# Kernel tuning notes

Measured on AMD Instinct MI355X. Metric: run time of the kernel, lower is better.

The kernel has to match this reference:

```python
import jax, jax.numpy as jnp
import numpy as np

B, T, D, UNITS = 32, 2048, 1024, 1024


def setup_inputs() -> dict:
    key = jax.random.key(0)
    ks = jax.random.split(key, 9)
    values = jax.random.normal(ks[0], (B, T, D), dtype=jnp.float32)
    query = jax.random.normal(ks[1], (B, D), dtype=jnp.float32)
    # mask: 1.0 where position is masked out, 0.0 otherwise
    mask = jax.random.randint(ks[2], (B, T), 0, 2).astype(jnp.float32)
    # Dense params (keras Dense: y = x @ W + b)
    W1 = jax.random.normal(ks[3], (D, UNITS), dtype=jnp.float32) / np.sqrt(D)
    b1 = jnp.zeros((UNITS,), dtype=jnp.float32)
    W2 = jax.random.normal(ks[4], (D, UNITS), dtype=jnp.float32) / np.sqrt(D)
    b2 = jnp.zeros((UNITS,), dtype=jnp.float32)
    V = jax.random.normal(ks[5], (UNITS, 1), dtype=jnp.float32) / np.sqrt(UNITS)
    bV = jnp.zeros((1,), dtype=jnp.float32)
    return {"values": values, "query": query, "mask": mask,
            "W1": W1, "b1": b1, "W2": W2, "b2": b2, "V": V, "bV": bV}


def reference(values, query, mask, W1, b1, W2, b2, V, bV):
    # values: [B,T,D], query: [B,D], mask: [B,T] (1.0 = masked)
    proj_v = jnp.einsum('btd,du->btu', values, W1) + b1          # [B,T,U]
    proj_q = (query @ W2 + b2)[:, None, :]                        # [B,1,U]
    score = jnp.tanh(proj_v + proj_q) @ V + bV                    # [B,T,1]
    score = score + mask[:, :, None] * (-1e9)                     # mask out
    attention_weights = jax.nn.softmax(score, axis=1)             # [B,T,1]
    context_vector = jnp.sum(attention_weights * values, axis=1)  # [B,D]
    return (context_vector, attention_weights)
```

## Files before the change

kernel.cpp:

```cpp
#include <hip/hip_runtime.h>
#include <hip/hip_bf16.h>


typedef __bf16 bf16x8 __attribute__((ext_vector_type(8)));
typedef __bf16 bf16x4 __attribute__((ext_vector_type(4)));
typedef float  f32x4  __attribute__((ext_vector_type(4)));

#define B_  32
#define T_  2048
#define D_  1024
#define U_  1024

#define WS_W1T    ((size_t)0)
#define WS_PROJQ  ((size_t)(2u*1024*1024))
#define WS_SCORE  ((size_t)(2u*1024*1024 + 128u*1024))

__global__ void init_kernel(const float* __restrict__ b1, const float* __restrict__ b2,
                            float* __restrict__ projq, float* __restrict__ score) {
    int i = blockIdx.x * 256 + threadIdx.x;
    if (i < B_ * U_) {
        projq[i] = b1[i & (U_ - 1)] + b2[i & (U_ - 1)];
    } else {
        score[i - B_ * U_] = 0.0f;
    }
}

__global__ void w1_transpose_kernel(const float* __restrict__ W1, __bf16* __restrict__ W1T) {
    __shared__ float tile[64][65];
    const int bx = blockIdx.x & 15;
    const int by = blockIdx.x >> 4;
    const int tid = threadIdx.x;
    const int j  = tid & 63;
    const int i0 = tid >> 6;
#pragma unroll
    for (int p = 0; p < 16; ++p) {
        const int i = i0 + p * 4;
        tile[i][j] = W1[(size_t)(by * 64 + i) * U_ + bx * 64 + j];
    }
    __syncthreads();
#pragma unroll
    for (int p = 0; p < 16; ++p) {
        const int i = i0 + p * 4;
        W1T[(size_t)(bx * 64 + i) * D_ + by * 64 + j] = (__bf16)tile[j][i];
    }
}

__global__ void projq_kernel(const float* __restrict__ query, const float* __restrict__ W2,
                             float* __restrict__ projq) {
    __shared__ float q[128];
    const int b  = blockIdx.x >> 3;
    const int dc = blockIdx.x & 7;
    const int tid = threadIdx.x;
    if (tid < 128) q[tid] = query[(size_t)b * D_ + dc * 128 + tid];
    __syncthreads();
    const int u0 = tid * 4;
    float a0 = 0.f, a1 = 0.f, a2 = 0.f, a3 = 0.f;
    for (int d = 0; d < 128; ++d) {
        const float4 w = *(const float4*)(W2 + (size_t)(dc * 128 + d) * U_ + u0);
        const float qd = q[d];
        a0 = fmaf(qd, w.x, a0); a1 = fmaf(qd, w.y, a1);
        a2 = fmaf(qd, w.z, a2); a3 = fmaf(qd, w.w, a3);
    }
    float* p = projq + (size_t)b * U_ + u0;
    atomicAdd(p + 0, a0); atomicAdd(p + 1, a1);
    atomicAdd(p + 2, a2); atomicAdd(p + 3, a3);
}

__global__ __launch_bounds__(512, 2)
void score_kernel(const float* __restrict__ values, const __bf16* __restrict__ W1T,
                  const float* __restrict__ projq, const float* __restrict__ V,
                  float* __restrict__ score) {
    __shared__ __attribute__((aligned(16))) __bf16 Al[64][40];
    __shared__ __attribute__((aligned(16))) __bf16 Bl[512][40];

    const int tid    = threadIdx.x;
    const int rowblk = blockIdx.x >> 1;
    const int nhalf  = blockIdx.x & 1;
    const int wave = tid >> 6, lane = tid & 63;
    const int quad = lane >> 4, l15 = lane & 15;

    const float*  Abase = values + (size_t)rowblk * 64 * D_;
    const __bf16* Bbase = W1T + (size_t)nhalf * 512 * D_;

    const int ar = tid >> 3;
    const int ac = (tid & 7) * 4;
    const int br = tid >> 2;
    const int bc = (tid & 3) * 8;

    f32x4 acc[4][4];
#pragma unroll
    for (int i = 0; i < 4; ++i)
#pragma unroll
        for (int j = 0; j < 4; ++j) {
            f32x4 z = {0.f, 0.f, 0.f, 0.f};
            acc[i][j] = z;
        }

    for (int kk = 0; kk < D_; kk += 32) {
        {
            const float4 v = *(const float4*)(Abase + (size_t)ar * D_ + kk + ac);
            bf16x4 h;
            h[0] = (__bf16)v.x; h[1] = (__bf16)v.y; h[2] = (__bf16)v.z; h[3] = (__bf16)v.w;
            *(bf16x4*)(&Al[ar][ac]) = h;
        }
#pragma unroll
        for (int p = 0; p < 4; ++p) {
            const int rr = p * 128 + br;
            const bf16x8 w = *(const bf16x8*)(Bbase + (size_t)rr * D_ + kk + bc);
            *(bf16x8*)(&Bl[rr][bc]) = w;
        }
        __syncthreads();

        bf16x8 af[4];
#pragma unroll
        for (int mt = 0; mt < 4; ++mt)
            af[mt] = *(const bf16x8*)(&Al[mt * 16 + l15][quad * 8]);
#pragma unroll
        for (int nt = 0; nt < 4; ++nt) {
            const bf16x8 bfr = *(const bf16x8*)(&Bl[wave * 64 + nt * 16 + l15][quad * 8]);
#pragma unroll
            for (int mt = 0; mt < 4; ++mt)
                acc[mt][nt] = __builtin_amdgcn_mfma_f32_16x16x32_bf16(af[mt], bfr, acc[mt][nt], 0, 0, 0);
        }
        __syncthreads();
    }

    const int b = rowblk >> 5;
    const size_t rowbase = (size_t)rowblk * 64;
    const float* pq = projq + (size_t)b * U_;
    const int ub = nhalf * 512 + wave * 64;
#pragma unroll
    for (int mt = 0; mt < 4; ++mt) {
        float s0 = 0.f, s1 = 0.f, s2 = 0.f, s3 = 0.f;
#pragma unroll
        for (int nt = 0; nt < 4; ++nt) {
            const int u = ub + nt * 16 + l15;
            const float pqu = pq[u];
            const float vu  = V[u];
            s0 += tanhf(acc[mt][nt][0] + pqu) * vu;
            s1 += tanhf(acc[mt][nt][1] + pqu) * vu;
            s2 += tanhf(acc[mt][nt][2] + pqu) * vu;
            s3 += tanhf(acc[mt][nt][3] + pqu) * vu;
        }
        float s[4] = {s0, s1, s2, s3};
#pragma unroll
        for (int r = 0; r < 4; ++r) {
            float v = s[r];
            v += __shfl_xor(v, 1);
            v += __shfl_xor(v, 2);
            v += __shfl_xor(v, 4);
            v += __shfl_xor(v, 8);
            if (l15 == 0)
                atomicAdd(&score[rowbase + mt * 16 + quad * 4 + r], v);
        }
    }
}

__global__ void softmax_kernel(const float* __restrict__ score, const float* __restrict__ mask,
                               const float* __restrict__ bV, float* __restrict__ out) {
    const int b = blockIdx.x;
    const int tid = threadIdx.x;
    const float bv = bV[0];
    float s[8];
    float lmax = -3.0e38f;
#pragma unroll
    for (int i = 0; i < 8; ++i) {
        const int t = tid + i * 256;
        const float v = score[(size_t)b * T_ + t] + bv + mask[(size_t)b * T_ + t] * (-1.0e9f);
        s[i] = v;
        lmax = fmaxf(lmax, v);
    }
#pragma unroll
    for (int m = 1; m < 64; m <<= 1) lmax = fmaxf(lmax, __shfl_xor(lmax, m));
    __shared__ float redm[4], reds[4];
    if ((tid & 63) == 0) redm[tid >> 6] = lmax;
    __syncthreads();
    const float M = fmaxf(fmaxf(redm[0], redm[1]), fmaxf(redm[2], redm[3]));
    float lsum = 0.f;
#pragma unroll
    for (int i = 0; i < 8; ++i) { s[i] = __expf(s[i] - M); lsum += s[i]; }
#pragma unroll
    for (int m = 1; m < 64; m <<= 1) lsum += __shfl_xor(lsum, m);
    if ((tid & 63) == 0) reds[tid >> 6] = lsum;
    __syncthreads();
    const float inv = 1.0f / (reds[0] + reds[1] + reds[2] + reds[3]);
#pragma unroll
    for (int i = 0; i < 8; ++i)
        out[(size_t)B_ * D_ + (size_t)b * T_ + tid + i * 256] = s[i] * inv;
}

__global__ void context_kernel(const float* __restrict__ values, const float* __restrict__ attn,
                               float* __restrict__ out) {
    const int b  = blockIdx.x >> 4;
    const int dc = blockIdx.x & 15;
    const int tid = threadIdx.x;
    __shared__ float a[T_];
#pragma unroll
    for (int i = 0; i < 8; ++i) a[tid + i * 256] = attn[(size_t)b * T_ + tid + i * 256];
    __syncthreads();
    const int d  = dc * 64 + (tid & 63);
    const int tg = tid >> 6;
    const float* vb = values + (size_t)b * T_ * D_ + d;
    float acc = 0.f;
#pragma unroll 4
    for (int t = tg; t < T_; t += 4)
        acc = fmaf(a[t], vb[(size_t)t * D_], acc);
    __shared__ float red[4][64];
    red[tg][tid & 63] = acc;
    __syncthreads();
    if (tid < 64)
        out[(size_t)b * D_ + dc * 64 + tid] = red[0][tid] + red[1][tid] + red[2][tid] + red[3][tid];
}

extern "C" void kernel_launch(void* const* d_in, const int* in_sizes, int n_in,
                              void* d_out, int out_size, void* d_ws, size_t ws_size,
                              hipStream_t stream) {
    const float* values = (const float*)d_in[0];
    const float* query  = (const float*)d_in[1];
    const float* mask   = (const float*)d_in[2];
    const float* W1     = (const float*)d_in[3];
    const float* b1     = (const float*)d_in[4];
    const float* W2     = (const float*)d_in[5];
    const float* b2     = (const float*)d_in[6];
    const float* V      = (const float*)d_in[7];
    const float* bV     = (const float*)d_in[8];
    float* out = (float*)d_out;

    char* ws = (char*)d_ws;
    __bf16* W1T  = (__bf16*)(ws + WS_W1T);
    float*  projq = (float*)(ws + WS_PROJQ);
    float*  score = (float*)(ws + WS_SCORE);

    init_kernel<<<dim3(384), dim3(256), 0, stream>>>(b1, b2, projq, score);
    w1_transpose_kernel<<<dim3(256), dim3(256), 0, stream>>>(W1, W1T);
    projq_kernel<<<dim3(256), dim3(256), 0, stream>>>(query, W2, projq);
    score_kernel<<<dim3(2048), dim3(512), 0, stream>>>(values, W1T, projq, V, score);
    softmax_kernel<<<dim3(32), dim3(256), 0, stream>>>(score, mask, bV, out);
    context_kernel<<<dim3(512), dim3(256), 0, stream>>>(values, out + B_ * D_, out);
}
```

Measured before the change: 714.3 us.

## Pre-convert values to bf16, retile score GEMM with direct-to-LDS loads, fast tanh

Adds a conversion pass that writes values as bf16 into workspace, then runs a new 128x128-tile score GEMM that loads A and B straight into LDS with global_load_lds. The previous f32-input kernel is kept as a fallback for when the workspace is too small. tanhf is replaced by an exp-based approximation. The context kernel is vectorised to float4 loads with 16 t-groups. The extra conversion pass adds a full read of values and a 128MB write, and the new path depends on the workspace size, which is not shown.

```diff
diff --git a/kernel.cpp b/kernel.cpp
--- a/kernel.cpp
+++ b/kernel.cpp
@@ -10,10 +10,24 @@
 #define T_  2048
 #define D_  1024
 #define U_  1024
+#define BT_ (B_*T_)
 
 #define WS_W1T    ((size_t)0)
 #define WS_PROJQ  ((size_t)(2u*1024*1024))
 #define WS_SCORE  ((size_t)(2u*1024*1024 + 128u*1024))
+#define WS_VALB   ((size_t)(4u*1024*1024))
+#define WS_NEEDED (WS_VALB + (size_t)BT_ * D_ * 2)
+
+__device__ __forceinline__ float tanh_fast(float x) {
+    const float e = __expf(2.0f * x);
+    return 1.0f - __fdividef(2.0f, e + 1.0f);
+}
+
+__device__ __forceinline__ void glls16(const void* g, void* l) {
+    __builtin_amdgcn_global_load_lds(
+        (const __attribute__((address_space(1))) void*)g,
+        (__attribute__((address_space(3))) void*)l, 16, 0, 0);
+}
 
 __global__ void init_kernel(const float* __restrict__ b1, const float* __restrict__ b2,
                             float* __restrict__ projq, float* __restrict__ score) {
@@ -25,6 +39,16 @@
     }
 }
 
+__global__ void convert_kernel(const float* __restrict__ v, __bf16* __restrict__ o) {
+    const size_t i = ((size_t)blockIdx.x * 256 + threadIdx.x) * 8;
+    const float4 a = *(const float4*)(v + i);
+    const float4 b = *(const float4*)(v + i + 4);
+    bf16x8 h;
+    h[0] = (__bf16)a.x; h[1] = (__bf16)a.y; h[2] = (__bf16)a.z; h[3] = (__bf16)a.w;
+    h[4] = (__bf16)b.x; h[5] = (__bf16)b.y; h[6] = (__bf16)b.z; h[7] = (__bf16)b.w;
+    *(bf16x8*)(o + i) = h;
+}
+
 __global__ void w1_transpose_kernel(const float* __restrict__ W1, __bf16* __restrict__ W1T) {
     __shared__ float tile[64][65];
     const int bx = blockIdx.x & 15;
@@ -66,26 +90,25 @@
     atomicAdd(p + 2, a2); atomicAdd(p + 3, a3);
 }
 
-__global__ __launch_bounds__(512, 2)
-void score_kernel(const float* __restrict__ values, const __bf16* __restrict__ W1T,
-                  const float* __restrict__ projq, const float* __restrict__ V,
-                  float* __restrict__ score) {
-    __shared__ __attribute__((aligned(16))) __bf16 Al[64][40];
-    __shared__ __attribute__((aligned(16))) __bf16 Bl[512][40];
-
-    const int tid    = threadIdx.x;
-    const int rowblk = blockIdx.x >> 1;
-    const int nhalf  = blockIdx.x & 1;
+__global__ __launch_bounds__(256, 3)
+void score_kernel_bf16(const __bf16* __restrict__ valb, const __bf16* __restrict__ W1T,
+                       const float* __restrict__ projq, const float* __restrict__ V,
+                       float* __restrict__ score) {
+    __shared__ __attribute__((aligned(16))) __bf16 Al[128 * 32];
+    __shared__ __attribute__((aligned(16))) __bf16 Bl[128 * 32];
+
+    const int tid = threadIdx.x;
+    const int rowblk = blockIdx.x >> 3;
+    const int utile  = blockIdx.x & 7;
     const int wave = tid >> 6, lane = tid & 63;
     const int quad = lane >> 4, l15 = lane & 15;
-
-    const float*  Abase = values + (size_t)rowblk * 64 * D_;
-    const __bf16* Bbase = W1T + (size_t)nhalf * 512 * D_;
-
-    const int ar = tid >> 3;
-    const int ac = (tid & 7) * 4;
-    const int br = tid >> 2;
-    const int bc = (tid & 3) * 8;
+    const int wr = (wave >> 1) * 64;
+    const int wc = (wave & 1) * 64;
+
+    const __bf16* Ab = valb + ((size_t)rowblk * 128 + (tid >> 2)) * D_ + (tid & 3) * 8;
+    const __bf16* Bb = W1T + ((size_t)utile * 128 + (tid >> 2)) * D_ + (tid & 3) * 8;
+    __bf16* Ald = Al + wave * 512;
+    __bf16* Bld = Bl + wave * 512;
 
     f32x4 acc[4][4];
 #pragma unroll
@@ -97,27 +120,19 @@
         }
 
     for (int kk = 0; kk < D_; kk += 32) {
-        {
-            const float4 v = *(const float4*)(Abase + (size_t)ar * D_ + kk + ac);
-            bf16x4 h;
-            h[0] = (__bf16)v.x; h[1] = (__bf16)v.y; h[2] = (__bf16)v.z; h[3] = (__bf16)v.w;
-            *(bf16x4*)(&Al[ar][ac]) = h;
-        }
-#pragma unroll
-        for (int p = 0; p < 4; ++p) {
-            const int rr = p * 128 + br;
-            const bf16x8 w = *(const bf16x8*)(Bbase + (size_t)rr * D_ + kk + bc);
-            *(bf16x8*)(&Bl[rr][bc]) = w;
-        }
+        glls16(Ab + kk,            Ald);
+        glls16(Ab + 64 * D_ + kk,  Ald + 2048);
+        glls16(Bb + kk,            Bld);
+        glls16(Bb + 64 * D_ + kk,  Bld + 2048);
         __syncthreads();
 
         bf16x8 af[4];
 #pragma unroll
         for (int mt = 0; mt < 4; ++mt)
-            af[mt] = *(const bf16x8*)(&Al[mt * 16 + l15][quad * 8]);
+            af[mt] = *(const bf16x8*)(Al + (wr + mt * 16 + l15) * 32 + quad * 8);
 #pragma unroll
         for (int nt = 0; nt < 4; ++nt) {
-            const bf16x8 bfr = *(const bf16x8*)(&Bl[wave * 64 + nt * 16 + l15][quad * 8]);
+            const bf16x8 bfr = *(const bf16x8*)(Bl + (wc + nt * 16 + l15) * 32 + quad * 8);
 #pragma unroll
             for (int mt = 0; mt < 4; ++mt)
                 acc[mt][nt] = __builtin_amdgcn_mfma_f32_16x16x32_bf16(af[mt], bfr, acc[mt][nt], 0, 0, 0);
@@ -125,22 +140,22 @@
         __syncthreads();
     }
 
-    const int b = rowblk >> 5;
-    const size_t rowbase = (size_t)rowblk * 64;
-    const float* pq = projq + (size_t)b * U_;
-    const int ub = nhalf * 512 + wave * 64;
+    const int b = rowblk >> 4;
+    const float* pq = projq + (size_t)b * U_ + utile * 128 + wc;
+    const float* Vp = V + utile * 128 + wc;
+    const size_t rowbase = (size_t)rowblk * 128 + wr;
 #pragma unroll
     for (int mt = 0; mt < 4; ++mt) {
         float s0 = 0.f, s1 = 0.f, s2 = 0.f, s3 = 0.f;
 #pragma unroll
         for (int nt = 0; nt < 4; ++nt) {
-            const int u = ub + nt * 16 + l15;
+            const int u = nt * 16 + l15;
             const float pqu = pq[u];
-            const float vu  = V[u];
-            s0 += tanhf(acc[mt][nt][0] + pqu) * vu;
-            s1 += tanhf(acc[mt][nt][1] + pqu) * vu;
-            s2 += tanhf(acc[mt][nt][2] + pqu) * vu;
-            s3 += tanhf(acc[mt][nt][3] + pqu) * vu;
+            const float vu  = Vp[u];
+            s0 += tanh_fast(acc[mt][nt][0] + pqu) * vu;
+            s1 += tanh_fast(acc[mt][nt][1] + pqu) * vu;
+            s2 += tanh_fast(acc[mt][nt][2] + pqu) * vu;
+            s3 += tanh_fast(acc[mt][nt][3] + pqu) * vu;
         }
         float s[4] = {s0, s1, s2, s3};
 #pragma unroll
@@ -156,6 +171,84 @@
     }
 }
 
+__global__ __launch_bounds__(512, 2)
+void score_kernel_f32(const float* __restrict__ values, const __bf16* __restrict__ W1T,
+                      const float* __restrict__ projq, const float* __restrict__ V,
+                      float* __restrict__ score) {
+    __shared__ __attribute__((aligned(16))) __bf16 Al[64][40];
+    __shared__ __attribute__((aligned(16))) __bf16 Bl[512][40];
+    const int tid    = threadIdx.x;
+    const int rowblk = blockIdx.x >> 1;
+    const int nhalf  = blockIdx.x & 1;
+    const int wave = tid >> 6, lane = tid & 63;
+    const int quad = lane >> 4, l15 = lane & 15;
+    const float*  Abase = values + (size_t)rowblk * 64 * D_;
+    const __bf16* Bbase = W1T + (size_t)nhalf * 512 * D_;
+    const int ar = tid >> 3, ac = (tid & 7) * 4;
+    const int br = tid >> 2, bc = (tid & 3) * 8;
+    f32x4 acc[4][4];
+#pragma unroll
+    for (int i = 0; i < 4; ++i)
+#pragma unroll
+        for (int j = 0; j < 4; ++j) { f32x4 z = {0.f,0.f,0.f,0.f}; acc[i][j] = z; }
+    for (int kk = 0; kk < D_; kk += 32) {
+        {
+            const float4 v = *(const float4*)(Abase + (size_t)ar * D_ + kk + ac);
+            bf16x4 h;
+            h[0] = (__bf16)v.x; h[1] = (__bf16)v.y; h[2] = (__bf16)v.z; h[3] = (__bf16)v.w;
+            *(bf16x4*)(&Al[ar][ac]) = h;
+        }
+#pragma unroll
+        for (int p = 0; p < 4; ++p) {
+            const int rr = p * 128 + br;
+            const bf16x8 w = *(const bf16x8*)(Bbase + (size_t)rr * D_ + kk + bc);
+            *(bf16x8*)(&Bl[rr][bc]) = w;
+        }
+        __syncthreads();
+        bf16x8 af[4];
+#pragma unroll
+        for (int mt = 0; mt < 4; ++mt)
+            af[mt] = *(const bf16x8*)(&Al[mt * 16 + l15][quad * 8]);
+#pragma unroll
+        for (int nt = 0; nt < 4; ++nt) {
+            const bf16x8 bfr = *(const bf16x8*)(&Bl[wave * 64 + nt * 16 + l15][quad * 8]);
+#pragma unroll
+            for (int mt = 0; mt < 4; ++mt)
+                acc[mt][nt] = __builtin_amdgcn_mfma_f32_16x16x32_bf16(af[mt], bfr, acc[mt][nt], 0, 0, 0);
+        }
+        __syncthreads();
+    }
+    const int b = rowblk >> 5;
+    const size_t rowbase = (size_t)rowblk * 64;
+    const float* pq = projq + (size_t)b * U_;
+    const int ub = nhalf * 512 + wave * 64;
+#pragma unroll
+    for (int mt = 0; mt < 4; ++mt) {
+        float s0 = 0.f, s1 = 0.f, s2 = 0.f, s3 = 0.f;
+#pragma unroll
+        for (int nt = 0; nt < 4; ++nt) {
+            const int u = ub + nt * 16 + l15;
+            const float pqu = pq[u];
+            const float vu  = V[u];
+            s0 += tanh_fast(acc[mt][nt][0] + pqu) * vu;
+            s1 += tanh_fast(acc[mt][nt][1] + pqu) * vu;
+            s2 += tanh_fast(acc[mt][nt][2] + pqu) * vu;
+            s3 += tanh_fast(acc[mt][nt][3] + pqu) * vu;
+        }
+        float s[4] = {s0, s1, s2, s3};
+#pragma unroll
+        for (int r = 0; r < 4; ++r) {
+            float v = s[r];
+            v += __shfl_xor(v, 1);
+            v += __shfl_xor(v, 2);
+            v += __shfl_xor(v, 4);
+            v += __shfl_xor(v, 8);
+            if (l15 == 0)
+                atomicAdd(&score[rowbase + mt * 16 + quad * 4 + r], v);
+        }
+    }
+}
+
 __global__ void softmax_kernel(const float* __restrict__ score, const float* __restrict__ mask,
                                const float* __restrict__ bV, float* __restrict__ out) {
     const int b = blockIdx.x;
@@ -198,18 +291,28 @@
 #pragma unroll
     for (int i = 0; i < 8; ++i) a[tid + i * 256] = attn[(size_t)b * T_ + tid + i * 256];
     __syncthreads();
-    const int d  = dc * 64 + (tid & 63);
-    const int tg = tid >> 6;
-    const float* vb = values + (size_t)b * T_ * D_ + d;
-    float acc = 0.f;
+    const int dl = (tid & 15) * 4;
+    const int tg = tid >> 4;
+    const float* vb = values + (size_t)b * T_ * D_ + dc * 64 + dl;
+    f32x4 acc = {0.f, 0.f, 0.f, 0.f};
 #pragma unroll 4
-    for (int t = tg; t < T_; t += 4)
-        acc = fmaf(a[t], vb[(size_t)t * D_], acc);
-    __shared__ float red[4][64];
-    red[tg][tid & 63] = acc;
-    __syncthreads();
-    if (tid < 64)
-        out[(size_t)b * D_ + dc * 64 + tid] = red[0][tid] + red[1][tid] + red[2][tid] + red[3][tid];
+    for (int t = tg; t < T_; t += 16) {
+        const float4 v = *(const float4*)(vb + (size_t)t * D_);
+        const float w = a[t];
+        acc[0] = fmaf(w, v.x, acc[0]);
+        acc[1] = fmaf(w, v.y, acc[1]);
+        acc[2] = fmaf(w, v.z, acc[2]);
+        acc[3] = fmaf(w, v.w, acc[3]);
+    }
+    __shared__ __attribute__((aligned(16))) float red[16][64];
+    *(f32x4*)(&red[tg][dl]) = acc;
+    __syncthreads();
+    if (tid < 64) {
+        float s = 0.f;
+#pragma unroll
+        for (int g = 0; g < 16; ++g) s += red[g][tid];
+        out[(size_t)b * D_ + dc * 64 + tid] = s;
+    }
 }
 
 extern "C" void kernel_launch(void* const* d_in, const int* in_sizes, int n_in,
@@ -227,14 +330,20 @@
     float* out = (float*)d_out;
 
     char* ws = (char*)d_ws;
-    __bf16* W1T  = (__bf16*)(ws + WS_W1T);
+    __bf16* W1T   = (__bf16*)(ws + WS_W1T);
     float*  projq = (float*)(ws + WS_PROJQ);
     float*  score = (float*)(ws + WS_SCORE);
+    __bf16* valb  = (__bf16*)(ws + WS_VALB);
 
     init_kernel<<<dim3(384), dim3(256), 0, stream>>>(b1, b2, projq, score);
     w1_transpose_kernel<<<dim3(256), dim3(256), 0, stream>>>(W1, W1T);
     projq_kernel<<<dim3(256), dim3(256), 0, stream>>>(query, W2, projq);
-    score_kernel<<<dim3(2048), dim3(512), 0, stream>>>(values, W1T, projq, V, score);
+    if (ws_size >= WS_NEEDED) {
+        convert_kernel<<<dim3(32768), dim3(256), 0, stream>>>(values, valb);
+        score_kernel_bf16<<<dim3(4096), dim3(256), 0, stream>>>(valb, W1T, projq, V, score);
+    } else {
+        score_kernel_f32<<<dim3(2048), dim3(512), 0, stream>>>(values, W1T, projq, V, score);
+    }
     softmax_kernel<<<dim3(32), dim3(256), 0, stream>>>(score, mask, bV, out);
     context_kernel<<<dim3(512), dim3(256), 0, stream>>>(values, out + B_ * D_, out);
 }
```

Result: faster. 641.5 us (-10.2%).
